# Kernel optimization log

Hardware: AMD Instinct MI355X
Metric: run time of the kernel (lower is better)

## Reference

```python
import jax, jax.numpy as jnp
import numpy as np

NUM_HEADS = 4
NUM_GROUPS = 8
EPS = 1e-5


def setup_inputs() -> dict:
    key = jax.random.key(0)
    ks = jax.random.split(key, 7)
    B, C, T, H, W = 2, 256, 16, 16, 16
    return {
        "x": jax.random.normal(ks[0], (B, C, T, H, W), dtype=jnp.float32),
        "norm_w": jax.random.normal(ks[1], (C,), dtype=jnp.float32),
        "norm_b": jax.random.normal(ks[2], (C,), dtype=jnp.float32),
        "qkv_w": jax.random.normal(ks[3], (3 * C, C), dtype=jnp.float32) * (C ** -0.5),
        "qkv_b": jax.random.normal(ks[4], (3 * C,), dtype=jnp.float32) * 0.02,
        "proj_w": jax.random.normal(ks[5], (C, C), dtype=jnp.float32) * (C ** -0.5),
        "proj_b": jax.random.normal(ks[6], (C,), dtype=jnp.float32) * 0.02,
    }


def reference(x, norm_w, norm_b, qkv_w, qkv_b, proj_w, proj_b):
    B, C, T, H, W = x.shape
    N = T * H * W
    hd = C // NUM_HEADS  # head dim

    # GroupNorm(8, C): stats over (C//G, T, H, W) per group
    xg = x.reshape(B, NUM_GROUPS, -1)
    mean = jnp.mean(xg, axis=-1, keepdims=True)
    var = jnp.var(xg, axis=-1, keepdims=True)
    xn = ((xg - mean) * jax.lax.rsqrt(var + EPS)).reshape(B, C, N)
    xn = xn * norm_w[None, :, None] + norm_b[None, :, None]

    # 1x1 conv3d qkv == per-token linear: (B, 3C, N)
    qkv = jnp.einsum('oc,bcn->bon', qkv_w, xn) + qkv_b[None, :, None]
    # reshape(B,3,heads,hd,N).permute(1,0,2,4,3) -> (3, B, heads, N, hd)
    qkv = qkv.reshape(B, 3, NUM_HEADS, hd, N).transpose(1, 0, 2, 4, 3)
    q, k, v = qkv[0], qkv[1], qkv[2]

    scale = hd ** -0.5
    scores = jnp.einsum('bhnd,bhmd->bhnm', q, k) * scale  # (B, heads, N, N)
    attn = jax.nn.softmax(scores, axis=-1)
    h = jnp.einsum('bhnm,bhmd->bhnd', attn, v)  # (B, heads, N, hd)

    # permute(0,1,3,2).reshape(B, C, T, H, W) -> channels-first tokens
    h = h.transpose(0, 1, 3, 2).reshape(B, C, N)
    out = jnp.einsum('oc,bcn->bon', proj_w, h) + proj_b[None, :, None]
    return out.reshape(B, C, T, H, W) + x
```

## Files before the change

### kernel.cpp

```cpp
#include <hip/hip_runtime.h>
#include <math.h>

#define B_DIM 2
#define C_DIM 256
#define N_TOK 4096
#define HEADS 4
#define HD 64
#define GROUPS 8
#define CPG (C_DIM / GROUPS)
#define EPS 1e-5f
#define PSB 72
#define QK_SCALE 0.180336880f
#define KSPLIT 4
#define NKT (N_TOK / 64)
#define QBLK 256
#define NQKVW (3 * C_DIM * C_DIM)
#define NPROJW (C_DIM * C_DIM)

typedef __bf16 bf16x8 __attribute__((ext_vector_type(8)));
typedef float  f32x4  __attribute__((ext_vector_type(4)));
typedef unsigned short u16x4v __attribute__((ext_vector_type(4)));
typedef unsigned short u16x8v __attribute__((ext_vector_type(8)));

__device__ __forceinline__ unsigned short f2bf(float f) {
    return __builtin_bit_cast(unsigned short, (__bf16)f);
}
__device__ __forceinline__ float bf2f(unsigned short u) {
    return (float)__builtin_bit_cast(__bf16, u);
}
__device__ __forceinline__ float exp2_fast(float x) { return __builtin_amdgcn_exp2f(x); }

__device__ __forceinline__ void gload16(const unsigned short* g, unsigned short* l) {
    __builtin_amdgcn_global_load_lds(
        (const __attribute__((address_space(1))) unsigned int*)g,
        (__attribute__((address_space(3))) unsigned int*)l, 16, 0, 0);
}

__device__ __forceinline__ int kperm(int r) {
    return (r & 0x23) | ((r & 0x0C) << 1) | ((r & 0x10) >> 2);
}

__global__ __launch_bounds__(256) void gn_part_kernel(const float* __restrict__ x,
                                                      const float* __restrict__ qkv_w,
                                                      const float* __restrict__ proj_w,
                                                      float* __restrict__ partials,
                                                      unsigned short* __restrict__ wbf) {
    const int bg = blockIdx.x >> 6, ch = blockIdx.x & 63;
    const float4* p = (const float4*)(x + (size_t)bg * CPG * N_TOK) + ch * 512;
    float s = 0.f, ss = 0.f;
#pragma unroll
    for (int r = 0; r < 2; ++r) {
        float4 v = p[threadIdx.x + (r << 8)];
        s  += v.x + v.y + v.z + v.w;
        ss += v.x * v.x + v.y * v.y + v.z * v.z + v.w * v.w;
    }
#pragma unroll
    for (int off = 32; off > 0; off >>= 1) {
        s  += __shfl_down(s, off);
        ss += __shfl_down(ss, off);
    }
    __shared__ float ls[4], lss[4];
    const int lane = threadIdx.x & 63, wid = threadIdx.x >> 6;
    if (lane == 0) { ls[wid] = s; lss[wid] = ss; }

    const int widx = blockIdx.x * 256 + threadIdx.x;
    float wv = (widx < NQKVW) ? qkv_w[widx] : proj_w[widx - NQKVW];
    wbf[widx] = f2bf(wv);

    __syncthreads();
    if (threadIdx.x == 0) {
        partials[blockIdx.x * 2 + 0] = ls[0] + ls[1] + ls[2] + ls[3];
        partials[blockIdx.x * 2 + 1] = lss[0] + lss[1] + lss[2] + lss[3];
    }
}

__global__ __launch_bounds__(256) void xnorm_kernel(const float* __restrict__ x,
                                                    const float* __restrict__ partials,
                                                    const float* __restrict__ norm_w,
                                                    const float* __restrict__ norm_b,
                                                    unsigned short* __restrict__ xnT) {
    __shared__ unsigned short Xt[64][PSB];
    __shared__ float stat_s[GROUPS][2];
    const int n0 = blockIdx.x * 64;
    const int c0 = blockIdx.y * 64;
    const int b  = blockIdx.z;
    const int tid = threadIdx.x;

    {
        const int g = tid >> 5, sub = tid & 31;
        const float* pp = partials + (((size_t)b * GROUPS + g) * 64 + sub * 2) * 2;
        float4 v = *(const float4*)pp;
        float s = v.x + v.z, ss = v.y + v.w;
#pragma unroll
        for (int off = 16; off > 0; off >>= 1) {
            s  += __shfl_down(s, off, 32);
            ss += __shfl_down(ss, off, 32);
        }
        if (sub == 0) {
            const float inv = 1.f / (float)(CPG * N_TOK);
            float mean = s * inv;
            float var  = ss * inv - mean * mean;
            stat_s[g][0] = mean;
            stat_s[g][1] = rsqrtf(var + EPS);
        }
        __syncthreads();
    }

#pragma unroll
    for (int r = 0; r < 4; ++r) {
        int idx = tid + (r << 8);
        int crow = idx >> 4, col4 = (idx & 15) << 2;
        int c = c0 + crow;
        int g = c >> 5;
        float ww = norm_w[c] * stat_s[g][1];
        float bb = norm_b[c] - stat_s[g][0] * ww;
        float4 v = *(const float4*)(x + ((size_t)b * C_DIM + c) * N_TOK + n0 + col4);
        Xt[col4 + 0][crow] = f2bf(v.x * ww + bb);
        Xt[col4 + 1][crow] = f2bf(v.y * ww + bb);
        Xt[col4 + 2][crow] = f2bf(v.z * ww + bb);
        Xt[col4 + 3][crow] = f2bf(v.w * ww + bb);
    }
    __syncthreads();

#pragma unroll
    for (int r = 0; r < 2; ++r) {
        int idx = tid + (r << 8);
        int row = idx >> 3, blk = idx & 7;
        *(u16x8v*)(xnT + ((size_t)b * N_TOK + n0 + row) * C_DIM + c0 + blk * 8) =
            *(const u16x8v*)&Xt[row][blk * 8];
    }
}

__global__ __launch_bounds__(256) void qkv_gemm_kernel(
    const unsigned short* __restrict__ xnT, const unsigned short* __restrict__ wqbf,
    const float* __restrict__ qkv_b, unsigned short* __restrict__ qkvb) {
    __shared__ unsigned short Ws[64][64];
    __shared__ unsigned short Xs[64][64];
    const int n0 = blockIdx.x * 64;
    const int o0 = blockIdx.y * 64;
    const int b  = blockIdx.z;
    const int tid = threadIdx.x;
    const int lane = tid & 63, w = tid >> 6;
    const int lo = lane & 15, hi = lane >> 4;
    const int srow8 = lane >> 3, sblk = lane & 7;
    const int c16s = (sblk ^ srow8) * 8;
    int rcol[2];
#pragma unroll
    for (int c = 0; c < 2; ++c) rcol[c] = (((c * 4 + hi) ^ (lo & 7)) << 3);

    f32x4 acc[4] = {};
    for (int k0 = 0; k0 < C_DIM; k0 += 64) {
#pragma unroll
        for (int i = 0; i < 2; ++i) {
            int row = i * 32 + w * 8 + srow8;
            gload16(wqbf + (size_t)(o0 + row) * C_DIM + k0 + c16s, &Ws[i * 32 + w * 8][0]);
            gload16(xnT + ((size_t)b * N_TOK + n0 + row) * C_DIM + k0 + c16s,
                    &Xs[i * 32 + w * 8][0]);
        }
        __syncthreads();
#pragma unroll
        for (int ck = 0; ck < 2; ++ck) {
            bf16x8 aw = *(const bf16x8*)&Ws[w * 16 + lo][rcol[ck]];
#pragma unroll
            for (int nb = 0; nb < 4; ++nb)
                acc[nb] = __builtin_amdgcn_mfma_f32_16x16x32_bf16(
                    aw, *(const bf16x8*)&Xs[nb * 16 + lo][rcol[ck]], acc[nb], 0, 0, 0);
        }
        __syncthreads();
    }

    const int sidx = o0 >> 8;
    const int head = (o0 >> 6) & 3;
    const int od = w * 16 + hi * 4;
    float bias[4];
#pragma unroll
    for (int i = 0; i < 4; ++i) bias[i] = qkv_b[o0 + od + i];
    const size_t plane = (size_t)N_TOK * HD;

    if (sidx < 2) {
        const float sc = (sidx == 0) ? QK_SCALE : 1.0f;
        unsigned short* base = qkvb + ((size_t)(sidx * B_DIM + b) * HEADS + head) * plane;
#pragma unroll
        for (int nb = 0; nb < 4; ++nb) {
            int n = n0 + nb * 16 + lo;
            u16x4v o;
#pragma unroll
            for (int i = 0; i < 4; ++i) o[i] = f2bf((acc[nb][i] + bias[i]) * sc);
            *(u16x4v*)(base + (size_t)n * HD + od) = o;
        }
    } else {
        unsigned short* base = qkvb + (size_t)2 * B_DIM * HEADS * plane
                             + ((size_t)b * HEADS + head) * plane;
#pragma unroll
        for (int nb = 0; nb < 4; ++nb)
#pragma unroll
            for (int i = 0; i < 4; ++i)
                base[(size_t)(od + i) * N_TOK + n0 + nb * 16 + lo] = f2bf(acc[nb][i] + bias[i]);
    }
}

__global__ __launch_bounds__(512, 4) void attn_kernel(const unsigned short* __restrict__ qkvb,
                                                      unsigned short* __restrict__ obuf,
                                                      float* __restrict__ rbuf) {
    const int bh = blockIdx.x & 7;
    const int ks = (blockIdx.x >> 3) & 3;
    const int q0 = (blockIdx.x >> 5) * QBLK;
    const size_t plane = (size_t)N_TOK * HD;
    const unsigned short* Qg  = qkvb + (size_t)bh * plane;
    const unsigned short* Kg  = qkvb + (size_t)(B_DIM * HEADS + bh) * plane;
    const unsigned short* Vtg = qkvb + (size_t)2 * B_DIM * HEADS * plane + (size_t)bh * plane;

    __shared__ unsigned short Ks[4][64][64];
    __shared__ unsigned short Vt[4][64][64];

    const int tid  = threadIdx.x;
    const int lane = tid & 63;
    const int wid  = tid >> 6;
    const int lo   = lane & 15;
    const int hi   = lane >> 4;

    bf16x8 qf[2][2];
#pragma unroll
    for (int f = 0; f < 2; ++f)
#pragma unroll
        for (int c = 0; c < 2; ++c)
            qf[f][c] = *(const bf16x8*)(Qg + (size_t)(q0 + wid * 32 + f * 16 + lo) * HD
                                            + c * 32 + hi * 8);

    const int srow = tid >> 3, sblk = tid & 7;
    const int c16s = (sblk ^ (srow & 7)) * 8;
    const int krow = kperm(srow);
    int rcol[2];
#pragma unroll
    for (int c = 0; c < 2; ++c) rcol[c] = (((c * 4 + hi) ^ (lo & 7)) << 3);

#define STAGE_KV(sloti, kbase)                                                         \
    do {                                                                               \
        gload16(Kg + (size_t)((kbase) + krow) * HD + c16s, &Ks[sloti][wid * 8][0]);    \
        gload16(Vtg + (size_t)srow * N_TOK + (kbase) + c16s, &Vt[sloti][wid * 8][0]);  \
    } while (0)

    const int kt0 = ks * (NKT / KSPLIT), ktE = kt0 + NKT / KSPLIT;

    f32x4 acc[2][4] = {};
    float m[2] = {-1e30f, -1e30f}, l[2] = {0.f, 0.f};

    auto compute_tile = [&](int cur) {
        f32x4 s4[2][4] = {};
        __builtin_amdgcn_s_setprio(1);
#pragma unroll
        for (int kb = 0; kb < 4; ++kb)
#pragma unroll
            for (int c = 0; c < 2; ++c) {
                bf16x8 kf = *(const bf16x8*)&Ks[cur][kb * 16 + lo][rcol[c]];
                s4[0][kb] = __builtin_amdgcn_mfma_f32_16x16x32_bf16(kf, qf[0][c], s4[0][kb], 0, 0, 0);
                s4[1][kb] = __builtin_amdgcn_mfma_f32_16x16x32_bf16(kf, qf[1][c], s4[1][kb], 0, 0, 0);
            }
        __builtin_amdgcn_s_setprio(0);

        bf16x8 pf[2][2];
#pragma unroll
        for (int f = 0; f < 2; ++f) {
            float r0 = fmaxf(fmaxf(fmaxf(s4[f][0][0], s4[f][0][1]), s4[f][0][2]), s4[f][0][3]);
            float r1 = fmaxf(fmaxf(fmaxf(s4[f][1][0], s4[f][1][1]), s4[f][1][2]), s4[f][1][3]);
            float r2 = fmaxf(fmaxf(fmaxf(s4[f][2][0], s4[f][2][1]), s4[f][2][2]), s4[f][2][3]);
            float r3 = fmaxf(fmaxf(fmaxf(s4[f][3][0], s4[f][3][1]), s4[f][3][2]), s4[f][3][3]);
            float rm = fmaxf(fmaxf(fmaxf(r0, r1), r2), r3);

            if (__any(rm > m[f] + 8.0f)) {
                float rmx = rm;
                rmx = fmaxf(rmx, __shfl_xor(rmx, 16));
                rmx = fmaxf(rmx, __shfl_xor(rmx, 32));
                const float mn = fmaxf(m[f], rmx);
                const float fi = exp2_fast(m[f] - mn);
                m[f] = mn;
                l[f] *= fi;
#pragma unroll
                for (int db = 0; db < 4; ++db)
#pragma unroll
                    for (int i = 0; i < 4; ++i) acc[f][db][i] *= fi;
            }

            float p[4][4];
            float ps = 0.f;
#pragma unroll
            for (int kb = 0; kb < 4; ++kb)
#pragma unroll
                for (int i = 0; i < 4; ++i) {
                    p[kb][i] = exp2_fast(s4[f][kb][i] - m[f]);
                    ps += p[kb][i];
                }
            l[f] += ps;

#pragma unroll
            for (int c = 0; c < 2; ++c)
#pragma unroll
                for (int j = 0; j < 8; ++j) pf[f][c][j] = (__bf16)p[2 * c + (j >> 2)][j & 3];
        }

        __builtin_amdgcn_s_setprio(1);
#pragma unroll
        for (int db = 0; db < 4; ++db)
#pragma unroll
            for (int c = 0; c < 2; ++c) {
                bf16x8 vf = *(const bf16x8*)&Vt[cur][db * 16 + lo][rcol[c]];
                acc[0][db] = __builtin_amdgcn_mfma_f32_16x16x32_bf16(vf, pf[0][c], acc[0][db], 0, 0, 0);
                acc[1][db] = __builtin_amdgcn_mfma_f32_16x16x32_bf16(vf, pf[1][c], acc[1][db], 0, 0, 0);
            }
        __builtin_amdgcn_s_setprio(0);
    };

    STAGE_KV(kt0 & 3, kt0 * 64);
    STAGE_KV((kt0 + 1) & 3, (kt0 + 1) * 64);
    __syncthreads();

    for (int kt = kt0; kt < ktE; kt += 2) {
        if (kt + 2 < ktE) {
            STAGE_KV((kt + 2) & 3, (kt + 2) * 64);
            STAGE_KV((kt + 3) & 3, (kt + 3) * 64);
        }
        compute_tile(kt & 3);
        compute_tile((kt + 1) & 3);
        __syncthreads();
    }
#undef STAGE_KV

#pragma unroll
    for (int f = 0; f < 2; ++f) {
        float l1 = l[f] + __shfl_xor(l[f], 16);
        float lt = l1 + __shfl_xor(l1, 32);
        const float inv = 1.f / lt;
        const int n = q0 + wid * 32 + f * 16 + lo;
        unsigned short* ob = obuf + ((size_t)(ks * 8 + bh) * N_TOK + n) * HD;
#pragma unroll
        for (int db = 0; db < 4; ++db) {
            u16x4v o;
#pragma unroll
            for (int i = 0; i < 4; ++i) o[i] = f2bf(acc[f][db][i] * inv);
            *(u16x4v*)(ob + db * 16 + hi * 4) = o;
        }
        if (hi == 0)
            rbuf[(size_t)(ks * 8 + bh) * N_TOK + n] = m[f] + __builtin_amdgcn_logf(lt);
    }
}

__global__ __launch_bounds__(256) void proj_kernel(
    const unsigned short* __restrict__ obuf, const float* __restrict__ rbuf,
    const unsigned short* __restrict__ wpbf, const float* __restrict__ proj_b,
    const float* __restrict__ x, float* __restrict__ out) {
    __shared__ unsigned short Ws[64][64];
    __shared__ unsigned short Hs[64][PSB];
    const int n0 = blockIdx.x * 64;
    const int o0 = blockIdx.y * 64;
    const int b  = blockIdx.z;
    const int tid = threadIdx.x;
    const int lane = tid & 63, w = tid >> 6;
    const int lo = lane & 15, hi = lane >> 4;
    const int srow8 = lane >> 3, sblk = lane & 7;
    const int c16s = (sblk ^ srow8) * 8;
    int rcol[2];
#pragma unroll
    for (int c = 0; c < 2; ++c) rcol[c] = (((c * 4 + hi) ^ (lo & 7)) << 3);

    f32x4 acc[4] = {};
    for (int k0 = 0; k0 < C_DIM; k0 += 64) {
#pragma unroll
        for (int i = 0; i < 2; ++i) {
            int row = i * 32 + w * 8 + srow8;
            gload16(wpbf + (size_t)(o0 + row) * C_DIM + k0 + c16s, &Ws[i * 32 + w * 8][0]);
        }
        {
            const int head = k0 >> 6;
            const int bh = b * HEADS + head;
#pragma unroll
            for (int r = 0; r < 2; ++r) {
                int idx = tid + (r << 8);
                int row = idx >> 3, blk = idx & 7;
                int n = n0 + row;
                float rr[KSPLIT], M = -1e30f;
#pragma unroll
                for (int k = 0; k < KSPLIT; ++k) {
                    rr[k] = rbuf[(size_t)(k * 8 + bh) * N_TOK + n];
                    M = fmaxf(M, rr[k]);
                }
                float wk[KSPLIT], tot = 0.f;
#pragma unroll
                for (int k = 0; k < KSPLIT; ++k) { wk[k] = exp2_fast(rr[k] - M); tot += wk[k]; }
                const float inv = 1.f / tot;
                float a[8] = {};
#pragma unroll
                for (int k = 0; k < KSPLIT; ++k) {
                    u16x8v v = *(const u16x8v*)(obuf
                        + ((size_t)(k * 8 + bh) * N_TOK + n) * HD + blk * 8);
#pragma unroll
                    for (int j = 0; j < 8; ++j) a[j] += wk[k] * bf2f(v[j]);
                }
                u16x8v o;
#pragma unroll
                for (int j = 0; j < 8; ++j) o[j] = f2bf(a[j] * inv);
                *(u16x8v*)&Hs[row][blk * 8] = o;
            }
        }
        __syncthreads();
#pragma unroll
        for (int ck = 0; ck < 2; ++ck) {
            bf16x8 aw = *(const bf16x8*)&Ws[w * 16 + lo][rcol[ck]];
#pragma unroll
            for (int nb = 0; nb < 4; ++nb)
                acc[nb] = __builtin_amdgcn_mfma_f32_16x16x32_bf16(
                    aw, *(const bf16x8*)&Hs[nb * 16 + lo][ck * 32 + hi * 8], acc[nb], 0, 0, 0);
        }
        __syncthreads();
    }

#pragma unroll
    for (int nb = 0; nb < 4; ++nb) {
#pragma unroll
        for (int i = 0; i < 4; ++i) {
            int o = o0 + w * 16 + hi * 4 + i;
            size_t addr = ((size_t)b * C_DIM + o) * N_TOK + n0 + nb * 16 + lo;
            out[addr] = acc[nb][i] + proj_b[o] + x[addr];
        }
    }
}

extern "C" void kernel_launch(void* const* d_in, const int* in_sizes, int n_in,
                              void* d_out, int out_size, void* d_ws, size_t ws_size,
                              hipStream_t stream) {
    const float* x      = (const float*)d_in[0];
    const float* norm_w = (const float*)d_in[1];
    const float* norm_b = (const float*)d_in[2];
    const float* qkv_w  = (const float*)d_in[3];
    const float* qkv_b  = (const float*)d_in[4];
    const float* proj_w = (const float*)d_in[5];
    const float* proj_b = (const float*)d_in[6];
    float* out = (float*)d_out;

    float* partials = (float*)d_ws;
    unsigned short* wbf = (unsigned short*)(partials + 2048);
    unsigned short* xnT = wbf + (NQKVW + NPROJW);
    unsigned short* qkvb = xnT + (size_t)B_DIM * N_TOK * C_DIM;
    unsigned short* obuf = qkvb + (size_t)3 * B_DIM * HEADS * N_TOK * HD;
    float* rbuf = (float*)(obuf + (size_t)KSPLIT * B_DIM * HEADS * N_TOK * HD);
    const unsigned short* wqbf = wbf;
    const unsigned short* wpbf = wbf + NQKVW;

    gn_part_kernel<<<B_DIM * GROUPS * 64, 256, 0, stream>>>(x, qkv_w, proj_w, partials, wbf);
    xnorm_kernel<<<dim3(N_TOK / 64, C_DIM / 64, B_DIM), 256, 0, stream>>>(
        x, partials, norm_w, norm_b, xnT);
    qkv_gemm_kernel<<<dim3(N_TOK / 64, 3 * C_DIM / 64, B_DIM), 256, 0, stream>>>(
        xnT, wqbf, qkv_b, qkvb);
    attn_kernel<<<(N_TOK / QBLK) * B_DIM * HEADS * KSPLIT, 512, 0, stream>>>(qkvb, obuf, rbuf);
    proj_kernel<<<dim3(N_TOK / 64, C_DIM / 64, B_DIM), 256, 0, stream>>>(
        obuf, rbuf, wpbf, proj_b, x, out);
}
```

Measured before the change: 78.83 us.

## Enlarge output-channel tiles in QKV and projection GEMMs with 512-thread blocks

The QKV GEMM now computes 256 output channels per block with 8 waves, each holding two 16-row fragments, so every X tile loaded to shared memory is reused across four times more weights. The projection GEMM now covers 128 output channels per block, which halves how often the expensive split-K attention merge (rbuf/obuf reads and rescaling) is recomputed per token tile. Grids shrink accordingly, giving fewer, larger blocks with more LDS and registers per block, which could lower occupancy and parallelism on a wide GPU.

New measurement: 78.05 us (median of 2 runs). About the same (-1.0%).

```diff
diff --git a/kernel.cpp b/kernel.cpp
--- a/kernel.cpp
+++ b/kernel.cpp
@@ -131,71 +131,81 @@
     }
 }
 
-__global__ __launch_bounds__(256) void qkv_gemm_kernel(
+__global__ __launch_bounds__(512) void qkv_gemm_kernel(
     const unsigned short* __restrict__ xnT, const unsigned short* __restrict__ wqbf,
     const float* __restrict__ qkv_b, unsigned short* __restrict__ qkvb) {
-    __shared__ unsigned short Ws[64][64];
+    __shared__ unsigned short Ws[256][64];
     __shared__ unsigned short Xs[64][64];
     const int n0 = blockIdx.x * 64;
-    const int o0 = blockIdx.y * 64;
+    const int o0 = blockIdx.y * 256;
     const int b  = blockIdx.z;
     const int tid = threadIdx.x;
     const int lane = tid & 63, w = tid >> 6;
     const int lo = lane & 15, hi = lane >> 4;
-    const int srow8 = lane >> 3, sblk = lane & 7;
-    const int c16s = (sblk ^ srow8) * 8;
+    const int tsrow = tid >> 3, tsblk = tid & 7;
+    const int tc16s = (tsblk ^ (tsrow & 7)) * 8;
     int rcol[2];
 #pragma unroll
     for (int c = 0; c < 2; ++c) rcol[c] = (((c * 4 + hi) ^ (lo & 7)) << 3);
 
-    f32x4 acc[4] = {};
+    f32x4 acc[2][4] = {};
     for (int k0 = 0; k0 < C_DIM; k0 += 64) {
 #pragma unroll
-        for (int i = 0; i < 2; ++i) {
-            int row = i * 32 + w * 8 + srow8;
-            gload16(wqbf + (size_t)(o0 + row) * C_DIM + k0 + c16s, &Ws[i * 32 + w * 8][0]);
-            gload16(xnT + ((size_t)b * N_TOK + n0 + row) * C_DIM + k0 + c16s,
-                    &Xs[i * 32 + w * 8][0]);
-        }
+        for (int i = 0; i < 4; ++i)
+            gload16(wqbf + (size_t)(o0 + i * 64 + tsrow) * C_DIM + k0 + tc16s,
+                    &Ws[i * 64 + w * 8][0]);
+        gload16(xnT + ((size_t)b * N_TOK + n0 + tsrow) * C_DIM + k0 + tc16s,
+                &Xs[w * 8][0]);
         __syncthreads();
 #pragma unroll
         for (int ck = 0; ck < 2; ++ck) {
-            bf16x8 aw = *(const bf16x8*)&Ws[w * 16 + lo][rcol[ck]];
-#pragma unroll
-            for (int nb = 0; nb < 4; ++nb)
-                acc[nb] = __builtin_amdgcn_mfma_f32_16x16x32_bf16(
-                    aw, *(const bf16x8*)&Xs[nb * 16 + lo][rcol[ck]], acc[nb], 0, 0, 0);
+            bf16x8 aw[2];
+#pragma unroll
+            for (int f = 0; f < 2; ++f)
+                aw[f] = *(const bf16x8*)&Ws[w * 32 + f * 16 + lo][rcol[ck]];
+#pragma unroll
+            for (int nb = 0; nb < 4; ++nb) {
+                bf16x8 xb = *(const bf16x8*)&Xs[nb * 16 + lo][rcol[ck]];
+                acc[0][nb] = __builtin_amdgcn_mfma_f32_16x16x32_bf16(aw[0], xb, acc[0][nb], 0, 0, 0);
+                acc[1][nb] = __builtin_amdgcn_mfma_f32_16x16x32_bf16(aw[1], xb, acc[1][nb], 0, 0, 0);
+            }
         }
         __syncthreads();
     }
 
     const int sidx = o0 >> 8;
-    const int head = (o0 >> 6) & 3;
-    const int od = w * 16 + hi * 4;
-    float bias[4];
-#pragma unroll
-    for (int i = 0; i < 4; ++i) bias[i] = qkv_b[o0 + od + i];
     const size_t plane = (size_t)N_TOK * HD;
-
-    if (sidx < 2) {
-        const float sc = (sidx == 0) ? QK_SCALE : 1.0f;
-        unsigned short* base = qkvb + ((size_t)(sidx * B_DIM + b) * HEADS + head) * plane;
-#pragma unroll
-        for (int nb = 0; nb < 4; ++nb) {
-            int n = n0 + nb * 16 + lo;
-            u16x4v o;
-#pragma unroll
-            for (int i = 0; i < 4; ++i) o[i] = f2bf((acc[nb][i] + bias[i]) * sc);
-            *(u16x4v*)(base + (size_t)n * HD + od) = o;
-        }
-    } else {
-        unsigned short* base = qkvb + (size_t)2 * B_DIM * HEADS * plane
-                             + ((size_t)b * HEADS + head) * plane;
-#pragma unroll
-        for (int nb = 0; nb < 4; ++nb)
-#pragma unroll
-            for (int i = 0; i < 4; ++i)
-                base[(size_t)(od + i) * N_TOK + n0 + nb * 16 + lo] = f2bf(acc[nb][i] + bias[i]);
+#pragma unroll
+    for (int f = 0; f < 2; ++f) {
+        const int ob = w * 32 + f * 16;
+        const int head = (ob >> 6) & 3;
+        const int od = (ob & 63) + hi * 4;
+        float bias[4];
+#pragma unroll
+        for (int i = 0; i < 4; ++i) bias[i] = qkv_b[o0 + ob + hi * 4 + i];
+
+        if (sidx < 2) {
+            const float sc = (sidx == 0) ? QK_SCALE : 1.0f;
+            unsigned short* base = qkvb + ((size_t)(sidx * B_DIM + b) * HEADS + head) * plane;
+#pragma unroll
+            for (int nb = 0; nb < 4; ++nb) {
+                int n = n0 + nb * 16 + lo;
+                u16x4v o;
+#pragma unroll
+                for (int i = 0; i < 4; ++i) o[i] = f2bf((acc[f][nb][i] + bias[i]) * sc);
+                *(u16x4v*)(base + (size_t)n * HD + od) = o;
+            }
+        } else {
+            unsigned short* base = qkvb + (size_t)2 * B_DIM * HEADS * plane
+                                 + ((size_t)b * HEADS + head) * plane;
+#pragma unroll
+            for (int nb = 0; nb < 4; ++nb) {
+                int n = n0 + nb * 16 + lo;
+#pragma unroll
+                for (int i = 0; i < 4; ++i)
+                    base[(size_t)(od + i) * N_TOK + n] = f2bf(acc[f][nb][i] + bias[i]);
+            }
+        }
     }
 }
 
@@ -344,20 +354,20 @@
     }
 }
 
-__global__ __launch_bounds__(256) void proj_kernel(
+__global__ __launch_bounds__(512) void proj_kernel(
     const unsigned short* __restrict__ obuf, const float* __restrict__ rbuf,
     const unsigned short* __restrict__ wpbf, const float* __restrict__ proj_b,
     const float* __restrict__ x, float* __restrict__ out) {
-    __shared__ unsigned short Ws[64][64];
+    __shared__ unsigned short Ws[128][64];
     __shared__ unsigned short Hs[64][PSB];
     const int n0 = blockIdx.x * 64;
-    const int o0 = blockIdx.y * 64;
+    const int o0 = blockIdx.y * 128;
     const int b  = blockIdx.z;
     const int tid = threadIdx.x;
     const int lane = tid & 63, w = tid >> 6;
     const int lo = lane & 15, hi = lane >> 4;
-    const int srow8 = lane >> 3, sblk = lane & 7;
-    const int c16s = (sblk ^ srow8) * 8;
+    const int tsrow = tid >> 3, tsblk = tid & 7;
+    const int tc16s = (tsblk ^ (tsrow & 7)) * 8;
     int rcol[2];
 #pragma unroll
     for (int c = 0; c < 2; ++c) rcol[c] = (((c * 4 + hi) ^ (lo & 7)) << 3);
@@ -365,41 +375,36 @@
     f32x4 acc[4] = {};
     for (int k0 = 0; k0 < C_DIM; k0 += 64) {
 #pragma unroll
-        for (int i = 0; i < 2; ++i) {
-            int row = i * 32 + w * 8 + srow8;
-            gload16(wpbf + (size_t)(o0 + row) * C_DIM + k0 + c16s, &Ws[i * 32 + w * 8][0]);
-        }
+        for (int i = 0; i < 2; ++i)
+            gload16(wpbf + (size_t)(o0 + i * 64 + tsrow) * C_DIM + k0 + tc16s,
+                    &Ws[i * 64 + w * 8][0]);
         {
             const int head = k0 >> 6;
             const int bh = b * HEADS + head;
-#pragma unroll
-            for (int r = 0; r < 2; ++r) {
-                int idx = tid + (r << 8);
-                int row = idx >> 3, blk = idx & 7;
-                int n = n0 + row;
-                float rr[KSPLIT], M = -1e30f;
-#pragma unroll
-                for (int k = 0; k < KSPLIT; ++k) {
-                    rr[k] = rbuf[(size_t)(k * 8 + bh) * N_TOK + n];
-                    M = fmaxf(M, rr[k]);
-                }
-                float wk[KSPLIT], tot = 0.f;
-#pragma unroll
-                for (int k = 0; k < KSPLIT; ++k) { wk[k] = exp2_fast(rr[k] - M); tot += wk[k]; }
-                const float inv = 1.f / tot;
-                float a[8] = {};
-#pragma unroll
-                for (int k = 0; k < KSPLIT; ++k) {
-                    u16x8v v = *(const u16x8v*)(obuf
-                        + ((size_t)(k * 8 + bh) * N_TOK + n) * HD + blk * 8);
-#pragma unroll
-                    for (int j = 0; j < 8; ++j) a[j] += wk[k] * bf2f(v[j]);
-                }
-                u16x8v o;
-#pragma unroll
-                for (int j = 0; j < 8; ++j) o[j] = f2bf(a[j] * inv);
-                *(u16x8v*)&Hs[row][blk * 8] = o;
-            }
+            int row = tsrow, blk = tsblk;
+            int n = n0 + row;
+            float rr[KSPLIT], M = -1e30f;
+#pragma unroll
+            for (int k = 0; k < KSPLIT; ++k) {
+                rr[k] = rbuf[(size_t)(k * 8 + bh) * N_TOK + n];
+                M = fmaxf(M, rr[k]);
+            }
+            float wk[KSPLIT], tot = 0.f;
+#pragma unroll
+            for (int k = 0; k < KSPLIT; ++k) { wk[k] = exp2_fast(rr[k] - M); tot += wk[k]; }
+            const float inv = 1.f / tot;
+            float a[8] = {};
+#pragma unroll
+            for (int k = 0; k < KSPLIT; ++k) {
+                u16x8v v = *(const u16x8v*)(obuf
+                    + ((size_t)(k * 8 + bh) * N_TOK + n) * HD + blk * 8);
+#pragma unroll
+                for (int j = 0; j < 8; ++j) a[j] += wk[k] * bf2f(v[j]);
+            }
+            u16x8v o;
+#pragma unroll
+            for (int j = 0; j < 8; ++j) o[j] = f2bf(a[j] * inv);
+            *(u16x8v*)&Hs[row][blk * 8] = o;
         }
         __syncthreads();
 #pragma unroll
@@ -448,9 +453,9 @@
     gn_part_kernel<<<B_DIM * GROUPS * 64, 256, 0, stream>>>(x, qkv_w, proj_w, partials, wbf);
     xnorm_kernel<<<dim3(N_TOK / 64, C_DIM / 64, B_DIM), 256, 0, stream>>>(
         x, partials, norm_w, norm_b, xnT);
-    qkv_gemm_kernel<<<dim3(N_TOK / 64, 3 * C_DIM / 64, B_DIM), 256, 0, stream>>>(
+    qkv_gemm_kernel<<<dim3(N_TOK / 64, 3, B_DIM), 512, 0, stream>>>(
         xnT, wqbf, qkv_b, qkvb);
     attn_kernel<<<(N_TOK / QBLK) * B_DIM * HEADS * KSPLIT, 512, 0, stream>>>(qkvb, obuf, rbuf);
-    proj_kernel<<<dim3(N_TOK / 64, C_DIM / 64, B_DIM), 256, 0, stream>>>(
+    proj_kernel<<<dim3(N_TOK / 64, 2, B_DIM), 512, 0, stream>>>(
         obuf, rbuf, wpbf, proj_b, x, out);
 }
```
